# Kernel tuning notes

Measured on AMD Instinct MI355X. Metric: run time of the kernel, lower is better.

## Reference

```python
import jax, jax.numpy as jnp
import numpy as np

HEADS = 8
DIM_HEAD = 64
SCALE = DIM_HEAD ** -0.5
K = 7


def _conv(x, w, stride):
    return jax.lax.conv_general_dilated(
        x, w, window_strides=(stride, stride), padding='VALID',
        dimension_numbers=('NHWC', 'HWIO', 'NHWC'))


def _split_heads(t):
    # 'b x y (h d) -> (b h) (x y) d'
    b, X, Y, hd = t.shape
    d = hd // HEADS
    t = t.reshape(b, X, Y, HEADS, d)
    t = t.transpose(0, 3, 1, 2, 4)  # b h x y d
    return t.reshape(b * HEADS, X * Y, d)


def setup_inputs() -> dict:
    key = jax.random.key(0)
    ks = jax.random.split(key, 6)
    dim, inner = 256, HEADS * DIM_HEAD
    x = jax.random.normal(ks[0], (8, 84, 84, dim), dtype=jnp.float32)
    w_q = jax.random.normal(ks[1], (1, 1, dim, inner), dtype=jnp.float32) * 0.02
    w_kv = jax.random.normal(ks[2], (K, K, dim, 2 * inner), dtype=jnp.float32) * 0.02
    w_out = jax.random.normal(ks[3], (1, 1, inner, dim), dtype=jnp.float32) * 0.02
    b_out = jnp.zeros((dim,), dtype=jnp.float32)
    return {"x": x, "w_q": w_q, "w_kv": w_kv, "w_out": w_out, "b_out": b_out}


def reference(x, w_q, w_kv, w_out, b_out):
    b, X, Y, _ = x.shape
    q = _conv(x, w_q, 1)          # [b, X, Y, inner]
    kv = _conv(x, w_kv, K)        # [b, X/k, Y/k, 2*inner]
    k, v = jnp.split(kv, 2, axis=-1)
    q = _split_heads(q)           # [(b h), XY, d]
    k = _split_heads(k)           # [(b h), xy, d]
    v = _split_heads(v)
    dots = jnp.einsum('bid,bjd->bij', q, k) * SCALE
    attn = jax.nn.softmax(dots, axis=-1)
    out = jnp.einsum('bij,bjd->bid', attn, v)  # [(b h), XY, d]
    out = out.reshape(b, HEADS, X, Y, DIM_HEAD).transpose(0, 2, 3, 1, 4)
    out = out.reshape(b, X, Y, HEADS * DIM_HEAD)
    out = _conv(out, w_out, 1) + b_out  # dropout rate 0 -> identity
    return out
```

## Files before the change

### kernel.cpp

```cpp
#include <hip/hip_runtime.h>

typedef unsigned short u16;
typedef __bf16 bf16x8 __attribute__((ext_vector_type(8)));
typedef __bf16 bf16x4 __attribute__((ext_vector_type(4)));
typedef float f32x4 __attribute__((ext_vector_type(4)));

__device__ __forceinline__ u16 f2b(float f) {
    __bf16 h = (__bf16)f;
    return __builtin_bit_cast(u16, h);
}

__device__ __forceinline__ int xcd_chunk(int wg, int n) {
    int q = n >> 3, r = n & 7;
    int x = wg & 7, i = wg >> 3;
    return (x < r ? x * (q + 1) : r * (q + 1) + (x - r) * q) + i;
}

#define GLOAD_LDS16(src, dst)                                              \
    __builtin_amdgcn_global_load_lds(                                      \
        (const __attribute__((address_space(1))) void*)(src),              \
        (__attribute__((address_space(3))) void*)(dst), 16, 0, 0)

__global__ __launch_bounds__(256) void k_pack_x(const float* __restrict__ x,
                                                u16* __restrict__ xp) {
    int v = blockIdx.x * 256 + threadIdx.x;
    int c0 = (v & 31) << 3;
    int pix = v >> 5;
    int b = pix / 7056;
    int r = pix - b * 7056;
    int y = r / 84;
    int xx = r - y * 84;
    int opix = (b * 144 + (y / 7) * 12 + (xx / 7)) * 49 + (y % 7) * 7 + (xx % 7);
    const float4* src = reinterpret_cast<const float4*>(x + ((size_t)pix << 8) + c0);
    float4 f0 = src[0], f1 = src[1];
    bf16x8 o = {(__bf16)f0.x, (__bf16)f0.y, (__bf16)f0.z, (__bf16)f0.w,
                (__bf16)f1.x, (__bf16)f1.y, (__bf16)f1.z, (__bf16)f1.w};
    *reinterpret_cast<bf16x8*>(xp + ((size_t)opix << 8) + c0) = o;
}

__global__ __launch_bounds__(256) void k_tconv(const float* __restrict__ in,
                                               u16* __restrict__ out, int R, int C,
                                               float scale, int permk) {
    __shared__ float tile[32][33];
    int c0 = blockIdx.x << 5, r0 = blockIdx.y << 5;
    int tx = threadIdx.x, ty = threadIdx.y;
#pragma unroll
    for (int i = 0; i < 4; i++)
        tile[ty + (i << 3)][tx] = in[(size_t)(r0 + ty + (i << 3)) * C + c0 + tx];
    __syncthreads();
    int k = r0 + tx;
    int kw = permk ? ((k & ~63) | ((k & 15) << 2) | ((k >> 4) & 3)) : k;
#pragma unroll
    for (int i = 0; i < 4; i++)
        out[(size_t)(c0 + ty + (i << 3)) * R + kw] = f2b(tile[tx][ty + (i << 3)] * scale);
}

__global__ __launch_bounds__(256) void k_kvproj(const u16* __restrict__ xp,
                                                const u16* __restrict__ wkvT,
                                                float* __restrict__ parts) {
    __shared__ u16 As[8192];
    __shared__ u16 Bs[8192];
    const int lin = xcd_chunk(blockIdx.x, 504);
    const int mt = lin % 9;
    const int ntsp = lin / 9;
    const int nt = ntsp & 7;
    const int sp = ntsp >> 3;
    const int tid = threadIdx.x;
    const int wave = tid >> 6, lane = tid & 63;
    const int wr = wave >> 1, wc = wave & 1;
    const int lrow = lane & 15, lkg = lane >> 4;
    const u16* Ag = xp + (size_t)(mt * 128) * 12544 + sp * 1792;
    const u16* Bg = wkvT + (size_t)(nt * 128) * 12544 + sp * 1792;
    const int srow = lane >> 3, scol = (lane & 7) << 3;
    f32x4 acc[4][4];
#pragma unroll
    for (int m = 0; m < 4; m++)
#pragma unroll
        for (int n = 0; n < 4; n++)
#pragma unroll
            for (int i = 0; i < 4; i++) acc[m][n][i] = 0.f;

    for (int ks = 0; ks < 28; ks++) {
        const int k0 = ks << 6;
        __syncthreads();
#pragma unroll
        for (int j = 0; j < 4; j++) {
            const int c = (wave << 2) + j;
            const int row = (c << 3) + srow;
            GLOAD_LDS16(Ag + (size_t)row * 12544 + k0 + scol, As + (c << 9));
            GLOAD_LDS16(Bg + (size_t)row * 12544 + k0 + scol, Bs + (c << 9));
        }
        __syncthreads();
#pragma unroll
        for (int kk = 0; kk < 2; kk++) {
            const int ko = (kk << 5) + (lkg << 3);
            bf16x8 a[4], bb[4];
#pragma unroll
            for (int m = 0; m < 4; m++)
                a[m] = *reinterpret_cast<const bf16x8*>(As + (((wr << 6) + (m << 4) + lrow) << 6) + ko);
#pragma unroll
            for (int n = 0; n < 4; n++)
                bb[n] = *reinterpret_cast<const bf16x8*>(Bs + (((wc << 6) + (n << 4) + lrow) << 6) + ko);
#pragma unroll
            for (int m = 0; m < 4; m++)
#pragma unroll
                for (int n = 0; n < 4; n++)
                    acc[m][n] = __builtin_amdgcn_mfma_f32_16x16x32_bf16(a[m], bb[n], acc[m][n], 0, 0, 0);
        }
    }
    float* outp = parts + (size_t)sp * 1179648;
#pragma unroll
    for (int m = 0; m < 4; m++)
#pragma unroll
        for (int n = 0; n < 4; n++)
#pragma unroll
            for (int i = 0; i < 4; i++) {
                int row = (mt << 7) + (wr << 6) + (m << 4) + (lkg << 2) + i;
                int col = (nt << 7) + (wc << 6) + (n << 4) + lrow;
                outp[(size_t)row * 1024 + col] = acc[m][n][i];
            }
}

__global__ __launch_bounds__(256) void k_kvfin(const float* __restrict__ parts,
                                               u16* __restrict__ Kf, u16* __restrict__ Vf) {
    int idx = blockIdx.x * 256 + threadIdx.x;
    int m = idx >> 10, n = idx & 1023;
    float s = 0.f;
#pragma unroll
    for (int sp = 0; sp < 7; sp++) s += parts[(size_t)sp * 1179648 + idx];
    int b = m / 144, pi = m - b * 144;
    int h = (n & 511) >> 6, d = n & 63;
    int bh = (b << 3) + h;
    if (n < 512) {
        int fc = pi >> 4, lr = pi & 15;
        int ks = d >> 5, lg = (d >> 3) & 3, e = d & 7;
        Kf[((((size_t)bh * 9 + fc) << 1) + ks) * 512 + (((lg << 4) + lr) << 3) + e] = f2b(s);
    } else {
        int nf = d >> 4, lr = d & 15;
        int ks = pi >> 5, lg = (pi >> 3) & 3, e = pi & 7;
        Vf[(((size_t)bh * 4 + nf) * 5 + ks) * 512 + (((lg << 4) + lr) << 3) + e] = f2b(s);
    }
}

__global__ __launch_bounds__(256) void k_qproj(const u16* __restrict__ xp,
                                               const u16* __restrict__ wqT,
                                               u16* __restrict__ Qf) {
    __shared__ u16 As[128][72];
    __shared__ u16 Bs[128][72];
    const int lin = xcd_chunk(blockIdx.x, 1764);
    const int nt = lin & 3, mt = lin >> 2;
    const int tid = threadIdx.x;
    const int wave = tid >> 6, lane = tid & 63;
    const int wr = wave >> 1, wc = wave & 1;
    const int lrow = lane & 15, lkg = lane >> 4;
    const u16* Ag = xp + (size_t)(mt * 128) * 256;
    const u16* Bg = wqT + (size_t)(nt * 128) * 256;
    const int srow = tid >> 3, scol = (tid & 7) << 3;
    f32x4 acc[4][4];
#pragma unroll
    for (int m = 0; m < 4; m++)
#pragma unroll
        for (int n = 0; n < 4; n++)
#pragma unroll
            for (int i = 0; i < 4; i++) acc[m][n][i] = 0.f;

    for (int ks = 0; ks < 4; ks++) {
        const int k0 = ks * 64;
        __syncthreads();
#pragma unroll
        for (int p = 0; p < 4; p++) {
            int rr = srow + (p << 5);
            *reinterpret_cast<bf16x8*>(&As[rr][scol]) =
                *reinterpret_cast<const bf16x8*>(Ag + (size_t)rr * 256 + k0 + scol);
            *reinterpret_cast<bf16x8*>(&Bs[rr][scol]) =
                *reinterpret_cast<const bf16x8*>(Bg + (size_t)rr * 256 + k0 + scol);
        }
        __syncthreads();
#pragma unroll
        for (int kk = 0; kk < 2; kk++) {
            const int ko = (kk << 5) + (lkg << 3);
            bf16x8 a[4], bb[4];
#pragma unroll
            for (int m = 0; m < 4; m++)
                a[m] = *reinterpret_cast<const bf16x8*>(&As[(wr << 6) + (m << 4) + lrow][ko]);
#pragma unroll
            for (int n = 0; n < 4; n++)
                bb[n] = *reinterpret_cast<const bf16x8*>(&Bs[(wc << 6) + (n << 4) + lrow][ko]);
#pragma unroll
            for (int m = 0; m < 4; m++)
#pragma unroll
                for (int n = 0; n < 4; n++)
                    acc[m][n] = __builtin_amdgcn_mfma_f32_16x16x32_bf16(a[m], bb[n], acc[m][n], 0, 0, 0);
        }
    }
#pragma unroll
    for (int m = 0; m < 4; m++)
#pragma unroll
        for (int n = 0; n < 4; n++)
#pragma unroll
            for (int i = 0; i < 4; i++) {
                int row = (mt << 7) + (wr << 6) + (m << 4) + (lkg << 2) + i;
                int col = (nt << 7) + (wc << 6) + (n << 4) + lrow;
                int b = row / 7056, pp = row - b * 7056;
                int h = col >> 6, d = col & 63;
                int bh = (b << 3) + h;
                int tt = pp >> 4, flr = pp & 15;
                int fks = d >> 5, flg = (d >> 3) & 3, fe = d & 7;
                Qf[((((size_t)bh * 441 + tt) << 1) + fks) * 512 + (((flg << 4) + flr) << 3) + fe] =
                    f2b(acc[m][n][i]);
            }
}

__global__ __launch_bounds__(128, 8) void k_attn(const u16* __restrict__ Qf,
                                                 const u16* __restrict__ Kf,
                                                 const u16* __restrict__ Vf,
                                                 u16* __restrict__ O) {
    __shared__ u16 smem[2 * 16 * 168];
    const int wv = threadIdx.x >> 6, lane = threadIdx.x & 63;
    const int t = blockIdx.x;
    const int h = (blockIdx.y << 1) + wv;
    const int b = blockIdx.z;
    const int lrow = lane & 15, lkg = lane >> 4;
    const int bh = (b << 3) + h;
    u16* sm = smem + wv * (16 * 168);
    const int l8 = lane << 3;

    const u16* Qg = Qf + ((((size_t)bh * 441 + t) << 1) << 9);
    const u16* Kg = Kf + (((size_t)bh * 9) << 10);
    const u16* Vg = Vf + ((size_t)bh * 20) * 512;

    f32x4 da[9];
#pragma unroll
    for (int fc = 0; fc < 9; fc++)
#pragma unroll
        for (int i = 0; i < 4; i++) da[fc][i] = 0.f;
#pragma unroll
    for (int ks = 0; ks < 2; ks++) {
        bf16x8 aq = *reinterpret_cast<const bf16x8*>(Qg + (ks << 9) + l8);
#pragma unroll
        for (int fc = 0; fc < 9; fc++) {
            bf16x8 bk = *reinterpret_cast<const bf16x8*>(Kg + ((((fc << 1) + ks)) << 9) + l8);
            da[fc] = __builtin_amdgcn_mfma_f32_16x16x32_bf16(aq, bk, da[fc], 0, 0, 0);
        }
    }

#pragma unroll
    for (int i = 0; i < 4; i++) {
        float mx = -1e30f;
#pragma unroll
        for (int fc = 0; fc < 9; fc++) mx = fmaxf(mx, da[fc][i]);
#pragma unroll
        for (int s = 1; s < 16; s <<= 1) mx = fmaxf(mx, __shfl_xor(mx, s));
        float e[9];
        float sum = 0.f;
#pragma unroll
        for (int fc = 0; fc < 9; fc++) {
            e[fc] = __expf(da[fc][i] - mx);
            sum += e[fc];
        }
#pragma unroll
        for (int s = 1; s < 16; s <<= 1) sum += __shfl_xor(sum, s);
        float inv = 1.0f / sum;
        int r = (lkg << 2) + i;
#pragma unroll
        for (int fc = 0; fc < 9; fc++) sm[r * 168 + (fc << 4) + lrow] = f2b(e[fc] * inv);
        sm[r * 168 + 144 + lrow] = 0;
    }
    asm volatile("" ::: "memory");

    f32x4 oa[4];
#pragma unroll
    for (int n = 0; n < 4; n++)
#pragma unroll
        for (int i = 0; i < 4; i++) oa[n][i] = 0.f;
#pragma unroll
    for (int ks = 0; ks < 5; ks++) {
        const int k0 = (ks << 5) + (lkg << 3);
        bf16x8 pa = *reinterpret_cast<const bf16x8*>(sm + (size_t)lrow * 168 + k0);
#pragma unroll
        for (int n = 0; n < 4; n++) {
            bf16x8 bv = *reinterpret_cast<const bf16x8*>(Vg + ((size_t)(n * 5 + ks) << 9) + l8);
            oa[n] = __builtin_amdgcn_mfma_f32_16x16x32_bf16(pa, bv, oa[n], 0, 0, 0);
        }
    }

#pragma unroll
    for (int i = 0; i < 4; i++) {
        int r = (lkg << 2) + i;
        int q = (t << 4) + r;
        int pi = q / 49, pos = q - pi * 49;
        int y = (pi / 12) * 7 + pos / 7;
        int xx = (pi - (pi / 12) * 12) * 7 + (pos - (pos / 7) * 7);
        bf16x4 ov = {(__bf16)oa[0][i], (__bf16)oa[1][i], (__bf16)oa[2][i], (__bf16)oa[3][i]};
        *reinterpret_cast<bf16x4*>(O + (((size_t)b * 7056 + y * 84 + xx) << 9) +
                                   (h << 6) + (lrow << 2)) = ov;
    }
}

__global__ __launch_bounds__(256) void k_outproj(const u16* __restrict__ A,
                                                 const u16* __restrict__ BT,
                                                 const float* __restrict__ bias,
                                                 float* __restrict__ out) {
    __shared__ u16 As[128][72];
    __shared__ u16 Bs[128][72];
    const int lin = xcd_chunk(blockIdx.x, 882);
    const int nt = lin & 1, mt = lin >> 1;
    const int tid = threadIdx.x;
    const int wave = tid >> 6, lane = tid & 63;
    const int wr = wave >> 1, wc = wave & 1;
    const int lrow = lane & 15, lkg = lane >> 4;
    const u16* Ag = A + (size_t)(mt * 128) * 512;
    const u16* Bg = BT + (size_t)(nt * 128) * 512;
    const int srow = tid >> 3, scol = (tid & 7) << 3;
    f32x4 acc[4][4];
#pragma unroll
    for (int m = 0; m < 4; m++)
#pragma unroll
        for (int n = 0; n < 4; n++)
#pragma unroll
            for (int i = 0; i < 4; i++) acc[m][n][i] = 0.f;

    for (int ks = 0; ks < 8; ks++) {
        const int k0 = ks * 64;
        __syncthreads();
#pragma unroll
        for (int p = 0; p < 4; p++) {
            int rr = srow + (p << 5);
            *reinterpret_cast<bf16x8*>(&As[rr][scol]) =
                *reinterpret_cast<const bf16x8*>(Ag + (size_t)rr * 512 + k0 + scol);
            *reinterpret_cast<bf16x8*>(&Bs[rr][scol]) =
                *reinterpret_cast<const bf16x8*>(Bg + (size_t)rr * 512 + k0 + scol);
        }
        __syncthreads();
#pragma unroll
        for (int kk = 0; kk < 2; kk++) {
            const int ko = (kk << 5) + (lkg << 3);
            bf16x8 a[4], bb[4];
#pragma unroll
            for (int m = 0; m < 4; m++)
                a[m] = *reinterpret_cast<const bf16x8*>(&As[(wr << 6) + (m << 4) + lrow][ko]);
#pragma unroll
            for (int n = 0; n < 4; n++)
                bb[n] = *reinterpret_cast<const bf16x8*>(&Bs[(wc << 6) + (n << 4) + lrow][ko]);
#pragma unroll
            for (int m = 0; m < 4; m++)
#pragma unroll
                for (int n = 0; n < 4; n++)
                    acc[m][n] = __builtin_amdgcn_mfma_f32_16x16x32_bf16(a[m], bb[n], acc[m][n], 0, 0, 0);
        }
    }
#pragma unroll
    for (int m = 0; m < 4; m++)
#pragma unroll
        for (int n = 0; n < 4; n++)
#pragma unroll
            for (int i = 0; i < 4; i++) {
                int row = (mt << 7) + (wr << 6) + (m << 4) + (lkg << 2) + i;
                int col = (nt << 7) + (wc << 6) + (n << 4) + lrow;
                out[(size_t)row * 256 + col] = acc[m][n][i] + bias[col];
            }
}

extern "C" void kernel_launch(void* const* d_in, const int* in_sizes, int n_in,
                              void* d_out, int out_size, void* d_ws, size_t ws_size,
                              hipStream_t stream) {
    const float* x = (const float*)d_in[0];
    const float* w_q = (const float*)d_in[1];
    const float* w_kv = (const float*)d_in[2];
    const float* w_out = (const float*)d_in[3];
    const float* b_out = (const float*)d_in[4];
    float* out = (float*)d_out;

    char* ws = (char*)d_ws;
    size_t off = 0;
    auto alloc = [&](size_t bytes) -> char* {
        char* p = ws + off;
        off = (off + bytes + 255) & ~(size_t)255;
        return p;
    };
    u16* xp = (u16*)alloc(28901376ull);
    u16* wqT = (u16*)alloc(262144ull);
    u16* woutT = (u16*)alloc(262144ull);
    u16* Kf = (u16*)alloc(1179648ull);
    u16* Vf = (u16*)alloc(1310720ull);
    u16* O = (u16*)alloc(57802752ull);
    u16* wkvT = (u16*)alloc(25690112ull);
    float* parts = (float*)alloc(33030144ull);
    u16* Qf = (u16*)wkvT;

    hipMemsetAsync(Vf, 0, 1310720ull, stream);
    k_pack_x<<<7056, 256, 0, stream>>>(x, xp);
    k_tconv<<<dim3(32, 392), dim3(32, 8), 0, stream>>>(w_kv, wkvT, 12544, 1024, 1.0f, 0);
    k_tconv<<<dim3(16, 8), dim3(32, 8), 0, stream>>>(w_q, wqT, 256, 512, 0.125f, 0);
    k_tconv<<<dim3(8, 16), dim3(32, 8), 0, stream>>>(w_out, woutT, 512, 256, 1.0f, 1);
    k_kvproj<<<504, 256, 0, stream>>>(xp, wkvT, parts);
    k_kvfin<<<4608, 256, 0, stream>>>(parts, Kf, Vf);
    k_qproj<<<1764, 256, 0, stream>>>(xp, wqT, Qf);
    k_attn<<<dim3(441, 4, 8), 128, 0, stream>>>(Qf, Kf, Vf, O);
    k_outproj<<<882, 256, 0, stream>>>(O, woutT, b_out, out);
}
```

Measured before the change: 229.9 us.

## Keep attention probabilities in registers by transposing QK MFMA and permuting V layout

Swaps the MFMA operand order for the score computation so each lane holds scores for a single query row across the key columns. The softmax then needs only two cross-lane shuffles instead of four per reduction. The bf16 probabilities are packed directly into the A operand of the PV MFMA, which removes the LDS staging buffer. To match this register layout, the V fragment layout in k_kvfin is permuted and the occupancy hint on the attention kernel is lowered.

```diff
diff --git a/kernel.cpp b/kernel.cpp
--- a/kernel.cpp
+++ b/kernel.cpp
@@ -8,6 +8,9 @@
 __device__ __forceinline__ u16 f2b(float f) {
     __bf16 h = (__bf16)f;
     return __builtin_bit_cast(u16, h);
+}
+__device__ __forceinline__ unsigned pk2(float a, float b) {
+    return (unsigned)f2b(a) | ((unsigned)f2b(b) << 16);
 }
 
 __device__ __forceinline__ int xcd_chunk(int wg, int n) {
@@ -137,7 +140,9 @@
         Kf[((((size_t)bh * 9 + fc) << 1) + ks) * 512 + (((lg << 4) + lr) << 3) + e] = f2b(s);
     } else {
         int nf = d >> 4, lr = d & 15;
-        int ks = pi >> 5, lg = (pi >> 3) & 3, e = pi & 7;
+        int ks = pi >> 5;
+        int e = (((pi >> 4) & 1) << 2) | (pi & 3);
+        int lg = (pi >> 2) & 3;
         Vf[(((size_t)bh * 4 + nf) * 5 + ks) * 512 + (((lg << 4) + lr) << 3) + e] = f2b(s);
     }
 }
@@ -211,18 +216,16 @@
             }
 }
 
-__global__ __launch_bounds__(128, 8) void k_attn(const u16* __restrict__ Qf,
+__global__ __launch_bounds__(128, 4) void k_attn(const u16* __restrict__ Qf,
                                                  const u16* __restrict__ Kf,
                                                  const u16* __restrict__ Vf,
                                                  u16* __restrict__ O) {
-    __shared__ u16 smem[2 * 16 * 168];
     const int wv = threadIdx.x >> 6, lane = threadIdx.x & 63;
     const int t = blockIdx.x;
     const int h = (blockIdx.y << 1) + wv;
     const int b = blockIdx.z;
     const int lrow = lane & 15, lkg = lane >> 4;
     const int bh = (b << 3) + h;
-    u16* sm = smem + wv * (16 * 168);
     const int l8 = lane << 3;
 
     const u16* Qg = Qf + ((((size_t)bh * 441 + t) << 1) << 9);
@@ -240,33 +243,35 @@
 #pragma unroll
         for (int fc = 0; fc < 9; fc++) {
             bf16x8 bk = *reinterpret_cast<const bf16x8*>(Kg + ((((fc << 1) + ks)) << 9) + l8);
-            da[fc] = __builtin_amdgcn_mfma_f32_16x16x32_bf16(aq, bk, da[fc], 0, 0, 0);
-        }
-    }
-
-#pragma unroll
-    for (int i = 0; i < 4; i++) {
-        float mx = -1e30f;
-#pragma unroll
-        for (int fc = 0; fc < 9; fc++) mx = fmaxf(mx, da[fc][i]);
-#pragma unroll
-        for (int s = 1; s < 16; s <<= 1) mx = fmaxf(mx, __shfl_xor(mx, s));
-        float e[9];
-        float sum = 0.f;
-#pragma unroll
-        for (int fc = 0; fc < 9; fc++) {
-            e[fc] = __expf(da[fc][i] - mx);
-            sum += e[fc];
-        }
-#pragma unroll
-        for (int s = 1; s < 16; s <<= 1) sum += __shfl_xor(sum, s);
-        float inv = 1.0f / sum;
-        int r = (lkg << 2) + i;
-#pragma unroll
-        for (int fc = 0; fc < 9; fc++) sm[r * 168 + (fc << 4) + lrow] = f2b(e[fc] * inv);
-        sm[r * 168 + 144 + lrow] = 0;
-    }
-    asm volatile("" ::: "memory");
+            da[fc] = __builtin_amdgcn_mfma_f32_16x16x32_bf16(bk, aq, da[fc], 0, 0, 0);
+        }
+    }
+
+    float mx = -1e30f;
+#pragma unroll
+    for (int fc = 0; fc < 9; fc++)
+#pragma unroll
+        for (int i = 0; i < 4; i++) mx = fmaxf(mx, da[fc][i]);
+    mx = fmaxf(mx, __shfl_xor(mx, 16));
+    mx = fmaxf(mx, __shfl_xor(mx, 32));
+    float sum = 0.f;
+#pragma unroll
+    for (int fc = 0; fc < 9; fc++)
+#pragma unroll
+        for (int i = 0; i < 4; i++) {
+            float v = __expf(da[fc][i] - mx);
+            da[fc][i] = v;
+            sum += v;
+        }
+    sum += __shfl_xor(sum, 16);
+    sum += __shfl_xor(sum, 32);
+    float inv = 1.0f / sum;
+    unsigned pw[9][2];
+#pragma unroll
+    for (int fc = 0; fc < 9; fc++) {
+        pw[fc][0] = pk2(da[fc][0] * inv, da[fc][1] * inv);
+        pw[fc][1] = pk2(da[fc][2] * inv, da[fc][3] * inv);
+    }
 
     f32x4 oa[4];
 #pragma unroll
@@ -275,8 +280,12 @@
         for (int i = 0; i < 4; i++) oa[n][i] = 0.f;
 #pragma unroll
     for (int ks = 0; ks < 5; ks++) {
-        const int k0 = (ks << 5) + (lkg << 3);
-        bf16x8 pa = *reinterpret_cast<const bf16x8*>(sm + (size_t)lrow * 168 + k0);
+        uint4 pav;
+        if (ks < 4)
+            pav = uint4{pw[2 * ks][0], pw[2 * ks][1], pw[2 * ks + 1][0], pw[2 * ks + 1][1]};
+        else
+            pav = uint4{pw[8][0], pw[8][1], 0u, 0u};
+        bf16x8 pa = __builtin_bit_cast(bf16x8, pav);
 #pragma unroll
         for (int n = 0; n < 4; n++) {
             bf16x8 bv = *reinterpret_cast<const bf16x8*>(Vg + ((size_t)(n * 5 + ks) << 9) + l8);
```

Measured after the change: 222.4 us. -3.3%, faster.
